# Kernel optimization log

Measured on AMD Instinct MI355X. Metric: run time of the kernel, lower is better.

## Reference

```python
import jax, jax.numpy as jnp
import numpy as np

N_HEADS = 16
KQ_DIM = 64
EMB_DIM = 1024
CTX_DIM = 1024
EPS = 1e-5

def _layernorm(x, w, b):
    # LayerNorm over last dim (kq_dim), elementwise affine
    mu = jnp.mean(x, axis=-1, keepdims=True)
    var = jnp.mean(jnp.square(x - mu), axis=-1, keepdims=True)
    return (x - mu) * jax.lax.rsqrt(var + EPS) * w + b

def setup_inputs() -> dict:
    key = jax.random.key(0)
    ks = jax.random.split(key, 10)
    B, SQ, SK = 2, 2048, 2048
    inner = N_HEADS * KQ_DIM
    s_e = 1.0 / np.sqrt(EMB_DIM)
    s_c = 1.0 / np.sqrt(CTX_DIM)
    s_i = 1.0 / np.sqrt(inner)
    return {
        "emb": jax.random.normal(ks[0], (B, SQ, EMB_DIM), jnp.float32),
        "context": jax.random.normal(ks[1], (B, SK, CTX_DIM), jnp.float32),
        "Wq": jax.random.uniform(ks[2], (inner, EMB_DIM), jnp.float32, -s_e, s_e),
        "Wk": jax.random.uniform(ks[3], (inner, CTX_DIM), jnp.float32, -s_c, s_c),
        "Wv": jax.random.uniform(ks[4], (inner, CTX_DIM), jnp.float32, -s_c, s_c),
        "Wu": jax.random.uniform(ks[5], (EMB_DIM, inner), jnp.float32, -s_i, s_i),
        "bu": jax.random.uniform(ks[6], (EMB_DIM,), jnp.float32, -s_i, s_i),
        "qn_w": jnp.ones((KQ_DIM,), jnp.float32),
        "qn_b": jnp.zeros((KQ_DIM,), jnp.float32),
        "kn_w": jnp.ones((KQ_DIM,), jnp.float32),
        "kn_b": jnp.zeros((KQ_DIM,), jnp.float32),
    }

def reference(emb, context, Wq, Wk, Wv, Wu, bu, qn_w, qn_b, kn_w, kn_b):
    B, SQ, _ = emb.shape
    SK = context.shape[1]
    # projections (no bias), reshape to [B, H, S, D]
    q = (emb @ Wq.T).reshape(B, SQ, N_HEADS, KQ_DIM).transpose(0, 2, 1, 3)
    k = (context @ Wk.T).reshape(B, SK, N_HEADS, KQ_DIM).transpose(0, 2, 1, 3)
    v = (context @ Wv.T).reshape(B, SK, N_HEADS, KQ_DIM).transpose(0, 2, 1, 3)
    q = _layernorm(q, qn_w, qn_b)
    k = _layernorm(k, kn_w, kn_b)
    scale = 1.0 / jnp.sqrt(jnp.asarray(KQ_DIM, emb.dtype))
    attn = jnp.einsum('bhqd,bhkd->bhqk', q, k) * scale
    attn = jax.nn.softmax(attn, axis=-1)
    out = jnp.einsum('bhqk,bhkd->bhqd', attn, v)
    out = out.transpose(0, 2, 1, 3).reshape(B, SQ, N_HEADS * KQ_DIM)
    return out @ Wu.T + bu
```

## Files before the change

### kernel.cpp

```cpp
#include <hip/hip_runtime.h>


typedef __attribute__((ext_vector_type(8)))  short bf16x8;
typedef __attribute__((ext_vector_type(4)))  short bf16x4;
typedef __attribute__((ext_vector_type(4)))  float f32x4;
typedef __attribute__((ext_vector_type(16))) float f32x16;
typedef __attribute__((ext_vector_type(4)))  unsigned int u32x4;

#define SM_SCALE 0.18033688f

typedef __attribute__((address_space(1))) const void cg_void;
typedef __attribute__((address_space(3))) void lds_void_t;

__device__ __forceinline__ void gl_lds16(const void* g, void* l){
  __builtin_amdgcn_global_load_lds((cg_void*)g, (lds_void_t*)l, 16, 0, 0);
}

__device__ __forceinline__ short f2b(float f){
  unsigned int u;
  __builtin_memcpy(&u, &f, 4);
  u += 0x7fffu + ((u >> 16) & 1u);
  return (short)(u >> 16);
}

__global__ __launch_bounds__(256) void cvt6_kernel(
    const float* __restrict__ emb, const float* __restrict__ ctx,
    const float* __restrict__ Wq, const float* __restrict__ Wk,
    const float* __restrict__ Wv, const float* __restrict__ Wu,
    short* __restrict__ o_emb, short* __restrict__ o_ctx,
    short* __restrict__ o_wq, short* __restrict__ o_wk,
    short* __restrict__ o_wv, short* __restrict__ o_wu)
{
  const long M1 = 1024L * 1024L, M4 = 4L * M1;
  long e = ((long)blockIdx.x * 256 + threadIdx.x) * 4;
  if (e >= 12L * M1) return;
  const float* src; short* dst; long off;
  if      (e <     M4)      { src = emb; dst = o_emb; off = e;           }
  else if (e < 2 * M4)      { src = ctx; dst = o_ctx; off = e - M4;      }
  else if (e < 2 * M4 + M1) { src = Wq;  dst = o_wq;  off = e - 2 * M4;  }
  else if (e < 2 * M4 + 2*M1){src = Wk;  dst = o_wk;  off = e - 2*M4 - M1;}
  else if (e < 2 * M4 + 3*M1){src = Wv;  dst = o_wv;  off = e - 2*M4 - 2*M1;}
  else                      { src = Wu;  dst = o_wu;  off = e - 2*M4 - 3*M1;}
  f32x4 v = *(const f32x4*)(src + off);
  bf16x4 o;
  o[0] = f2b(v[0]); o[1] = f2b(v[1]); o[2] = f2b(v[2]); o[3] = f2b(v[3]);
  *(bf16x4*)(dst + off) = o;
}

__global__ __launch_bounds__(256, 3) void gemm_qkv_kernel(
    const short* __restrict__ embh, const short* __restrict__ ctxh,
    const short* __restrict__ Wqh, const short* __restrict__ Wkh,
    const short* __restrict__ Wvh,
    short* __restrict__ qo, short* __restrict__ ko, short* __restrict__ vto,
    const float* __restrict__ qw, const float* __restrict__ qb,
    const float* __restrict__ kw, const float* __restrict__ kb)
{
  const int K = 1024;
  __shared__ short As[128 * 64];
  __shared__ short Bs[128 * 64];
  const int tid  = threadIdx.x;
  const int wave = tid >> 6, lane = tid & 63;
  const int quad = lane >> 4, r16 = lane & 15;
  const int wm = (wave >> 1) * 64, wn = (wave & 1) * 64;

  const int task = blockIdx.y;
  int bn, bm, N;
  const short *A, *B;
  if (task == 2){
    bn = (blockIdx.x & 31) * 128; bm = (blockIdx.x >> 5) * 128; N = 4096;
    A = Wvh; B = ctxh;
  } else {
    bm = (blockIdx.x & 31) * 128; bn = (blockIdx.x >> 5) * 128; N = 1024;
    A = task ? ctxh : embh; B = task ? Wkh : Wqh;
  }

  f32x4 acc[4][4];
#pragma unroll
  for (int i = 0; i < 4; i++)
#pragma unroll
    for (int j = 0; j < 4; j++)
      acc[i][j] = (f32x4){0.f, 0.f, 0.f, 0.f};

  const int sr7 = (lane >> 3) & 7;
  const size_t arow = (size_t)(bm + wave * 8 + (lane >> 3)) * K
                      + (((lane & 7) ^ sr7) * 8);
  const size_t brow = (size_t)(bn + wave * 8 + (lane >> 3)) * K
                      + (((lane & 7) ^ sr7) * 8);
  const int sw = ((quad ^ (r16 & 7)) << 3);

  for (int k0 = 0; k0 < K; k0 += 64){
#pragma unroll
    for (int i = 0; i < 4; i++)
      gl_lds16(A + arow + (size_t)32 * i * K + k0, &As[wave * 512 + i * 2048]);
#pragma unroll
    for (int i = 0; i < 4; i++)
      gl_lds16(B + brow + (size_t)32 * i * K + k0, &Bs[wave * 512 + i * 2048]);
    __syncthreads();
#pragma unroll
    for (int kk = 0; kk < 2; kk++){
      const int off = sw ^ (kk << 5);
      bf16x8 af[4], bq[4];
#pragma unroll
      for (int i = 0; i < 4; i++)
        af[i] = *(const bf16x8*)(&As[(wm + i*16 + r16) * 64 + off]);
#pragma unroll
      for (int j = 0; j < 4; j++)
        bq[j] = *(const bf16x8*)(&Bs[(wn + j*16 + r16) * 64 + off]);
#pragma unroll
      for (int i = 0; i < 4; i++)
#pragma unroll
        for (int j = 0; j < 4; j++)
          acc[i][j] = __builtin_amdgcn_mfma_f32_16x16x32_bf16(af[i], bq[j], acc[i][j], 0, 0, 0);
    }
    __syncthreads();
  }

  if (task < 2){
    short* Ch = task ? ko : qo;
    const float* lw = task ? kw : qw;
    const float* lb = task ? kb : qb;
    const float post = task ? 1.0f : SM_SCALE;
    float wv[4], bv[4];
#pragma unroll
    for (int j = 0; j < 4; j++){
      wv[j] = lw[j*16 + r16] * post;
      bv[j] = lb[j*16 + r16] * post;
    }
#pragma unroll
    for (int i = 0; i < 4; i++){
#pragma unroll
      for (int t = 0; t < 4; t++){
        float a[4];
#pragma unroll
        for (int j = 0; j < 4; j++) a[j] = acc[i][j][t];
        float s = a[0] + a[1] + a[2] + a[3];
        s += __shfl_xor(s, 1); s += __shfl_xor(s, 2);
        s += __shfl_xor(s, 4); s += __shfl_xor(s, 8);
        const float mu = s * 0.015625f;
        float d[4], sq = 0.f;
#pragma unroll
        for (int j = 0; j < 4; j++){ d[j] = a[j] - mu; sq += d[j]*d[j]; }
        sq += __shfl_xor(sq, 1); sq += __shfl_xor(sq, 2);
        sq += __shfl_xor(sq, 4); sq += __shfl_xor(sq, 8);
        const float si = rsqrtf(sq * 0.015625f + 1e-5f);
        const size_t row = (size_t)(bm + wm + i*16 + quad*4 + t);
#pragma unroll
        for (int j = 0; j < 4; j++)
          Ch[row * 1024 + (bn + wn + j*16 + r16)] = f2b(d[j] * si * wv[j] + bv[j]);
      }
    }
  } else {
#pragma unroll
    for (int i = 0; i < 4; i++){
#pragma unroll
      for (int j = 0; j < 4; j++){
        const int p = (r16 & 3) | ((j & 1) << 2) | (((r16 >> 2) & 1) << 3)
                      | (((r16 >> 3) & 1) << 4);
        const int col = ((bn + wn + j*16 + r16) & ~31) | p;
#pragma unroll
        for (int t = 0; t < 4; t++){
          const size_t row = (size_t)(bm + wm + i*16 + quad*4 + t);
          vto[row * (size_t)N + col] = f2b(acc[i][j][t]);
        }
      }
    }
  }
}

__global__ __launch_bounds__(256, 4) void gemm_out_kernel(
    const short* __restrict__ A, const short* __restrict__ B,
    float* __restrict__ Cf, const float* __restrict__ bias)
{
  const int K = 1024, N = 1024;
  __shared__ short As[64 * 64];
  __shared__ short Bs[64 * 64];
  const int tid  = threadIdx.x;
  const int wave = tid >> 6, lane = tid & 63;
  const int quad = lane >> 4, r16 = lane & 15;
  const int wm = (wave >> 1) * 32, wn = (wave & 1) * 32;
  const int bm = blockIdx.x * 64, bn = blockIdx.y * 64;

  f32x4 acc[2][2];
#pragma unroll
  for (int i = 0; i < 2; i++)
#pragma unroll
    for (int j = 0; j < 2; j++)
      acc[i][j] = (f32x4){0.f, 0.f, 0.f, 0.f};

  const int sr7 = (lane >> 3) & 7;
  const size_t arow = (size_t)(bm + wave * 8 + (lane >> 3)) * K
                      + (((lane & 7) ^ sr7) * 8);
  const size_t brow = (size_t)(bn + wave * 8 + (lane >> 3)) * K
                      + (((lane & 7) ^ sr7) * 8);
  const int sw = ((quad ^ (r16 & 7)) << 3);

  for (int k0 = 0; k0 < K; k0 += 64){
#pragma unroll
    for (int i = 0; i < 2; i++){
      gl_lds16(A + arow + (size_t)32 * i * K + k0, &As[wave * 512 + i * 2048]);
      gl_lds16(B + brow + (size_t)32 * i * K + k0, &Bs[wave * 512 + i * 2048]);
    }
    __syncthreads();
#pragma unroll
    for (int kk = 0; kk < 2; kk++){
      const int off = sw ^ (kk << 5);
      bf16x8 af[2], bq[2];
#pragma unroll
      for (int i = 0; i < 2; i++)
        af[i] = *(const bf16x8*)(&As[(wm + i*16 + r16) * 64 + off]);
#pragma unroll
      for (int j = 0; j < 2; j++)
        bq[j] = *(const bf16x8*)(&Bs[(wn + j*16 + r16) * 64 + off]);
#pragma unroll
      for (int i = 0; i < 2; i++)
#pragma unroll
        for (int j = 0; j < 2; j++)
          acc[i][j] = __builtin_amdgcn_mfma_f32_16x16x32_bf16(af[i], bq[j], acc[i][j], 0, 0, 0);
    }
    __syncthreads();
  }

#pragma unroll
  for (int i = 0; i < 2; i++){
#pragma unroll
    for (int j = 0; j < 2; j++){
      const int col = bn + wn + j*16 + r16;
#pragma unroll
      for (int t = 0; t < 4; t++){
        const size_t row = (size_t)(bm + wm + i*16 + quad*4 + t);
        Cf[row * N + col] = acc[i][j][t] + bias[col];
      }
    }
  }
}

__global__ __launch_bounds__(256, 2) void flash2_kernel(
    const short* __restrict__ Q, const short* __restrict__ K,
    const short* __restrict__ Vt, short* __restrict__ O)
{
  __shared__ __align__(16) long long smem8[8192];
  short* Ks  = (short*)smem8;
  short* Vts = Ks + 16384;
  float* scr = (float*)smem8;

  const int tid = threadIdx.x;
  const int wave = tid >> 6, lane = tid & 63;
  const int half = wave >> 1, wg = wave & 1;
  const int hh = lane >> 5, q5 = lane & 31;
  const int h = blockIdx.x, qb = blockIdx.y, b = blockIdx.z;
  const int q0 = qb * 128 + wg * 64;

  const size_t kbase = ((size_t)b * 2048) * 1024 + (size_t)h * 64;
  const size_t vbase = ((size_t)h * 64) * 4096 + (size_t)b * 2048;

  bf16x8 qf[2][4];
#pragma unroll
  for (int qg = 0; qg < 2; qg++){
    const size_t qrow = ((size_t)b * 2048 + q0 + qg * 32 + q5) * 1024 + (size_t)h * 64;
#pragma unroll
    for (int c = 0; c < 4; c++)
      qf[qg][c] = *(const bf16x8*)(Q + qrow + c * 16 + hh * 8);
  }

  f32x16 oacc[2][2];
#pragma unroll
  for (int t = 0; t < 16; t++){
    oacc[0][0][t] = 0.f; oacc[0][1][t] = 0.f;
    oacc[1][0][t] = 0.f; oacc[1][1][t] = 0.f;
  }
  float lacc[2] = {0.f, 0.f};

  const int srow = lane >> 3;
  const int csrc = ((lane & 7) ^ srow) * 8;
  const int wr0 = wg * 32;

#define STAGE(bufi, kt)                                                         \
  {                                                                             \
    const short* ks = K + kbase + (size_t)((kt) * 64 + wr0 + srow) * 1024 + csrc; \
    const short* vs = Vt + vbase + (size_t)(wr0 + srow) * 4096 + (kt) * 64 + csrc; \
    short* kd = Ks  + (half * 2 + (bufi)) * 4096 + wr0 * 64;                    \
    short* vd = Vts + (half * 2 + (bufi)) * 4096 + wr0 * 64;                    \
    gl_lds16(ks,             kd);                                               \
    gl_lds16(ks +  8 * 1024, kd + 512);                                         \
    gl_lds16(ks + 16 * 1024, kd + 1024);                                        \
    gl_lds16(ks + 24 * 1024, kd + 1536);                                        \
    gl_lds16(vs,             vd);                                               \
    gl_lds16(vs +  8 * 4096, vd + 512);                                         \
    gl_lds16(vs + 16 * 4096, vd + 1024);                                        \
    gl_lds16(vs + 24 * 4096, vd + 1536);                                        \
  }

  STAGE(0, half)

  for (int i = 0; i < 16; i++){
    const int buf = i & 1;
    __syncthreads();
    if (i + 1 < 16) STAGE(buf ^ 1, 2 * (i + 1) + half)

    const short* kb_l = Ks  + (half * 2 + buf) * 4096;
    const short* vb_l = Vts + (half * 2 + buf) * 4096;

    bf16x8 kf[2][4];
#pragma unroll
    for (int s32 = 0; s32 < 2; s32++){
      const int key = s32 * 32 + q5;
#pragma unroll
      for (int c = 0; c < 4; c++)
        kf[s32][c] = *(const bf16x8*)(&kb_l[key * 64 + (((2*c + hh) ^ (key & 7)) << 3)]);
    }

    f32x16 sacc[2][2];
#pragma unroll
    for (int t = 0; t < 16; t++){
      sacc[0][0][t] = 0.f; sacc[0][1][t] = 0.f;
      sacc[1][0][t] = 0.f; sacc[1][1][t] = 0.f;
    }
#pragma unroll
    for (int c = 0; c < 4; c++){
      sacc[0][0] = __builtin_amdgcn_mfma_f32_32x32x16_bf16(kf[0][c], qf[0][c], sacc[0][0], 0, 0, 0);
      sacc[0][1] = __builtin_amdgcn_mfma_f32_32x32x16_bf16(kf[1][c], qf[0][c], sacc[0][1], 0, 0, 0);
      sacc[1][0] = __builtin_amdgcn_mfma_f32_32x32x16_bf16(kf[0][c], qf[1][c], sacc[1][0], 0, 0, 0);
      sacc[1][1] = __builtin_amdgcn_mfma_f32_32x32x16_bf16(kf[1][c], qf[1][c], sacc[1][1], 0, 0, 0);
    }

    bf16x8 pf[2][2][2];
#pragma unroll
    for (int qg = 0; qg < 2; qg++){
#pragma unroll
      for (int s32 = 0; s32 < 2; s32++){
        unsigned int pu[16];
        float pp[4] = {0.f, 0.f, 0.f, 0.f};
#pragma unroll
        for (int t = 0; t < 16; t++){
          const float e = __builtin_amdgcn_exp2f(sacc[qg][s32][t]);
          pp[t & 3] += e;
          unsigned int u; __builtin_memcpy(&u, &e, 4);
          pu[t] = u + 0x8000u;
        }
        lacc[qg] += (pp[0] + pp[1]) + (pp[2] + pp[3]);
#pragma unroll
        for (int c = 0; c < 2; c++){
          u32x4 tmp;
          tmp[0] = __builtin_amdgcn_perm(pu[4*c + 1], pu[4*c + 0], 0x07060302u);
          tmp[1] = __builtin_amdgcn_perm(pu[4*c + 3], pu[4*c + 2], 0x07060302u);
          tmp[2] = __builtin_amdgcn_perm(pu[8 + 4*c + 1], pu[8 + 4*c + 0], 0x07060302u);
          tmp[3] = __builtin_amdgcn_perm(pu[8 + 4*c + 3], pu[8 + 4*c + 2], 0x07060302u);
          __builtin_memcpy(&pf[qg][s32][c], &tmp, 16);
        }
      }
    }

#pragma unroll
    for (int s32 = 0; s32 < 2; s32++){
#pragma unroll
      for (int c = 0; c < 2; c++){
#pragma unroll
        for (int mt = 0; mt < 2; mt++){
          const int d = mt * 32 + q5;
          bf16x8 vf = *(const bf16x8*)(&vb_l[d * 64 + (((s32*4 + 2*c + hh) ^ (d & 7)) << 3)]);
          oacc[0][mt] = __builtin_amdgcn_mfma_f32_32x32x16_bf16(vf, pf[0][s32][c], oacc[0][mt], 0, 0, 0);
          oacc[1][mt] = __builtin_amdgcn_mfma_f32_32x32x16_bf16(vf, pf[1][s32][c], oacc[1][mt], 0, 0, 0);
        }
      }
    }
  }

  const int widx = wg * 64 + lane;
  __syncthreads();
#pragma unroll
  for (int qg = 0; qg < 2; qg++){
    const float lh = lacc[qg] + __shfl_xor(lacc[qg], 32);
    if (half == 1){
      float* base = scr + widx * 33;
#pragma unroll
      for (int t = 0; t < 16; t++){ base[t] = oacc[qg][0][t]; base[16 + t] = oacc[qg][1][t]; }
      scr[4224 + widx] = lh;
    }
    __syncthreads();
    if (half == 0){
      const float* base = scr + widx * 33;
      const float l2 = scr[4224 + widx];
      const float linv = 1.0f / (lh + l2);
      const size_t orow = ((size_t)b * 2048 + q0 + qg * 32 + q5) * 1024 + (size_t)h * 64;
#pragma unroll
      for (int mt = 0; mt < 2; mt++){
#pragma unroll
        for (int g = 0; g < 4; g++){
          bf16x4 o4;
#pragma unroll
          for (int u = 0; u < 4; u++)
            o4[u] = f2b((oacc[qg][mt][g*4 + u] + base[mt*16 + g*4 + u]) * linv);
          *(bf16x4*)(O + orow + mt*32 + g*8 + 4*hh) = o4;
        }
      }
    }
    __syncthreads();
  }
}
#undef STAGE

extern "C" void kernel_launch(void* const* d_in, const int* in_sizes, int n_in,
                              void* d_out, int out_size, void* d_ws, size_t ws_size,
                              hipStream_t stream) {
  const float* emb  = (const float*)d_in[0];
  const float* ctx  = (const float*)d_in[1];
  const float* Wq   = (const float*)d_in[2];
  const float* Wk   = (const float*)d_in[3];
  const float* Wv   = (const float*)d_in[4];
  const float* Wu   = (const float*)d_in[5];
  const float* bu   = (const float*)d_in[6];
  const float* qn_w = (const float*)d_in[7];
  const float* qn_b = (const float*)d_in[8];
  const float* kn_w = (const float*)d_in[9];
  const float* kn_b = (const float*)d_in[10];
  float* out = (float*)d_out;

  const size_t BIG = (size_t)4096 * 1024;
  const size_t WSZ = (size_t)1024 * 1024;
  short* ws   = (short*)d_ws;
  short* embh = ws;
  short* ctxh = embh + BIG;
  short* Wqh  = ctxh + BIG;
  short* Wkh  = Wqh + WSZ;
  short* Wvh  = Wkh + WSZ;
  short* Wuh  = Wvh + WSZ;
  short* qh   = Wuh + WSZ;
  short* kh   = qh + BIG;
  short* vth  = kh + BIG;
  short* aoh  = vth + BIG;

  cvt6_kernel<<<12288, 256, 0, stream>>>(emb, ctx, Wq, Wk, Wv, Wu,
                                         embh, ctxh, Wqh, Wkh, Wvh, Wuh);

  gemm_qkv_kernel<<<dim3(256, 3), 256, 0, stream>>>(
      embh, ctxh, Wqh, Wkh, Wvh, qh, kh, vth,
      qn_w, qn_b, kn_w, kn_b);

  flash2_kernel<<<dim3(16, 16, 2), 256, 0, stream>>>(qh, kh, vth, aoh);

  gemm_out_kernel<<<dim3(64, 16), 256, 0, stream>>>(aoh, Wuh, out, bu);
}
```

Measured before the change: 190.8 us.

## Store V in MFMA-fragment order and load V fragments directly from global

The QKV GEMM epilogue now writes V in a per-(batch, head, key-tile) layout that matches the exact MFMA operand fragment order for each lane. The flash attention kernel then loads V fragments straight from global memory with contiguous 16-byte per-lane reads, no longer staging V through LDS. This halves the LDS footprint, which could raise occupancy, and cuts LDS traffic and bank work. In exchange, V loads are issued within the iteration and their global latency is exposed, and the epilogue stores become scattered writes.

After: 190.4 us (median of 2 runs). Within noise of the previous version (-0.2%).

```diff
diff --git a/kernel.cpp b/kernel.cpp
--- a/kernel.cpp
+++ b/kernel.cpp
@@ -64,13 +64,13 @@
   const int wm = (wave >> 1) * 64, wn = (wave & 1) * 64;
 
   const int task = blockIdx.y;
-  int bn, bm, N;
+  int bn, bm;
   const short *A, *B;
   if (task == 2){
-    bn = (blockIdx.x & 31) * 128; bm = (blockIdx.x >> 5) * 128; N = 4096;
+    bn = (blockIdx.x & 31) * 128; bm = (blockIdx.x >> 5) * 128;
     A = Wvh; B = ctxh;
   } else {
-    bm = (blockIdx.x & 31) * 128; bn = (blockIdx.x >> 5) * 128; N = 1024;
+    bm = (blockIdx.x & 31) * 128; bn = (blockIdx.x >> 5) * 128;
     A = task ? ctxh : embh; B = task ? Wkh : Wqh;
   }
 
@@ -153,14 +153,22 @@
 #pragma unroll
     for (int i = 0; i < 4; i++){
 #pragma unroll
-      for (int j = 0; j < 4; j++){
-        const int p = (r16 & 3) | ((j & 1) << 2) | (((r16 >> 2) & 1) << 3)
-                      | (((r16 >> 3) & 1) << 4);
-        const int col = ((bn + wn + j*16 + r16) & ~31) | p;
+      for (int j4 = 0; j4 < 4; j4++){
 #pragma unroll
         for (int t = 0; t < 4; t++){
-          const size_t row = (size_t)(bm + wm + i*16 + quad*4 + t);
-          vto[row * (size_t)N + col] = f2b(acc[i][j][t]);
+          const int row  = bm + wm + i*16 + quad*4 + t;
+          const int col0 = bn + wn + j4*16 + r16;
+          const int bb  = col0 >> 11, tok = col0 & 2047;
+          const int hq  = row >> 6,  dd  = row & 63;
+          const int mt  = dd >> 5,   q5l = dd & 31;
+          const int kt  = tok >> 6,  tk  = tok & 63;
+          const int s32 = (tk >> 5) & 1, ks = tk & 31;
+          const int hi  = ks >> 4,   r   = ks & 15;
+          const int cc  = r >> 3, hh2 = (r >> 2) & 1, jj = (r & 3) + 4*hi;
+          const size_t addr = ((size_t)(bb*16 + hq) * 32 + kt) * 4096
+                            + (size_t)(((mt*2 + s32)*2 + cc) * 512)
+                            + (hh2*32 + q5l) * 8 + jj;
+          vto[addr] = f2b(acc[i][j4][t]);
         }
       }
     }
@@ -238,9 +246,8 @@
     const short* __restrict__ Q, const short* __restrict__ K,
     const short* __restrict__ Vt, short* __restrict__ O)
 {
-  __shared__ __align__(16) long long smem8[8192];
-  short* Ks  = (short*)smem8;
-  short* Vts = Ks + 16384;
+  __shared__ __align__(16) long long smem8[4096];
+  short* Ks = (short*)smem8;
   float* scr = (float*)smem8;
 
   const int tid = threadIdx.x;
@@ -251,7 +258,7 @@
   const int q0 = qb * 128 + wg * 64;
 
   const size_t kbase = ((size_t)b * 2048) * 1024 + (size_t)h * 64;
-  const size_t vbase = ((size_t)h * 64) * 4096 + (size_t)b * 2048;
+  const short* vbh = Vt + ((size_t)(b * 16 + h)) * 131072;
 
   bf16x8 qf[2][4];
 #pragma unroll
@@ -277,17 +284,11 @@
 #define STAGE(bufi, kt)                                                         \
   {                                                                             \
     const short* ks = K + kbase + (size_t)((kt) * 64 + wr0 + srow) * 1024 + csrc; \
-    const short* vs = Vt + vbase + (size_t)(wr0 + srow) * 4096 + (kt) * 64 + csrc; \
-    short* kd = Ks  + (half * 2 + (bufi)) * 4096 + wr0 * 64;                    \
-    short* vd = Vts + (half * 2 + (bufi)) * 4096 + wr0 * 64;                    \
+    short* kd = Ks + (half * 2 + (bufi)) * 4096 + wr0 * 64;                     \
     gl_lds16(ks,             kd);                                               \
     gl_lds16(ks +  8 * 1024, kd + 512);                                         \
     gl_lds16(ks + 16 * 1024, kd + 1024);                                        \
     gl_lds16(ks + 24 * 1024, kd + 1536);                                        \
-    gl_lds16(vs,             vd);                                               \
-    gl_lds16(vs +  8 * 4096, vd + 512);                                         \
-    gl_lds16(vs + 16 * 4096, vd + 1024);                                        \
-    gl_lds16(vs + 24 * 4096, vd + 1536);                                        \
   }
 
   STAGE(0, half)
@@ -297,8 +298,19 @@
     __syncthreads();
     if (i + 1 < 16) STAGE(buf ^ 1, 2 * (i + 1) + half)
 
-    const short* kb_l = Ks  + (half * 2 + buf) * 4096;
-    const short* vb_l = Vts + (half * 2 + buf) * 4096;
+    const int ktc = 2 * i + half;
+
+    bf16x8 vfr[2][2][2];
+#pragma unroll
+    for (int s32 = 0; s32 < 2; s32++)
+#pragma unroll
+      for (int c = 0; c < 2; c++)
+#pragma unroll
+        for (int mt = 0; mt < 2; mt++)
+          vfr[s32][c][mt] = *(const bf16x8*)(
+              vbh + (size_t)ktc * 4096 + (((mt*2 + s32)*2 + c) * 512) + lane * 8);
+
+    const short* kb_l = Ks + (half * 2 + buf) * 4096;
 
     bf16x8 kf[2][4];
 #pragma unroll
@@ -356,10 +368,8 @@
       for (int c = 0; c < 2; c++){
 #pragma unroll
         for (int mt = 0; mt < 2; mt++){
-          const int d = mt * 32 + q5;
-          bf16x8 vf = *(const bf16x8*)(&vb_l[d * 64 + (((s32*4 + 2*c + hh) ^ (d & 7)) << 3)]);
-          oacc[0][mt] = __builtin_amdgcn_mfma_f32_32x32x16_bf16(vf, pf[0][s32][c], oacc[0][mt], 0, 0, 0);
-          oacc[1][mt] = __builtin_amdgcn_mfma_f32_32x32x16_bf16(vf, pf[1][s32][c], oacc[1][mt], 0, 0, 0);
+          oacc[0][mt] = __builtin_amdgcn_mfma_f32_32x32x16_bf16(vfr[s32][c][mt], pf[0][s32][c], oacc[0][mt], 0, 0, 0);
+          oacc[1][mt] = __builtin_amdgcn_mfma_f32_32x32x16_bf16(vfr[s32][c][mt], pf[1][s32][c], oacc[1][mt], 0, 0, 0);
         }
       }
     }
```
